# Optimization experiments

Hardware: AMD Instinct MI355X
Metric: run time of the kernel (lower is better)

Reference implementation:

```python
import jax, jax.numpy as jnp
import numpy as np


def _rnn_scan(x_pre, W_hh, b_hh, h0):
    # x_pre: [S, B, H] precomputed input projection; returns stacked h: [S, B, H]
    def step(h, xp):
        h = jnp.tanh(xp + h @ W_hh.T + b_hh)
        return h, h
    _, hs = jax.lax.scan(step, h0, x_pre)
    return hs


def setup_inputs() -> dict:
    key = jax.random.key(0)
    ks = jax.random.split(key, 12)
    B, S, E, H, V = 16, 256, 512, 1024, 32000
    sE, sH = 1.0 / np.sqrt(E), 1.0 / np.sqrt(H)
    return {
        "x_ids": jax.random.randint(ks[0], (B, S), 0, V),
        "emb": jax.random.normal(ks[1], (V, E), jnp.float32),
        "W_ih1": jax.random.normal(ks[2], (H, E), jnp.float32) * sE,
        "b_ih1": jax.random.normal(ks[3], (H,), jnp.float32) * sH,
        "W_hh1": jax.random.normal(ks[4], (H, H), jnp.float32) * sH,
        "b_hh1": jax.random.normal(ks[5], (H,), jnp.float32) * sH,
        "W_ih2": jax.random.normal(ks[6], (H, H), jnp.float32) * sH,
        "b_ih2": jax.random.normal(ks[7], (H,), jnp.float32) * sH,
        "W_hh2": jax.random.normal(ks[8], (H, H), jnp.float32) * sH,
        "b_hh2": jax.random.normal(ks[9], (H,), jnp.float32) * sH,
        "W_fc": jax.random.normal(ks[10], (V, H), jnp.float32) * sH,
        "b_fc": jax.random.normal(ks[11], (V,), jnp.float32) * sH,
    }


def reference(x_ids, emb, W_ih1, b_ih1, W_hh1, b_hh1, W_ih2, b_ih2, W_hh2, b_hh2, W_fc, b_fc):
    B, S = x_ids.shape
    H = W_hh1.shape[0]
    x = emb[x_ids]  # [B, S, E]
    # layer 1: precompute input projection for all steps, scan over time
    x1 = jnp.einsum('bse,he->sbh', x, W_ih1) + b_ih1  # [S, B, H]
    h0 = jnp.zeros((B, H), x.dtype)
    h1s = _rnn_scan(x1, W_hh1, b_hh1, h0)  # [S, B, H]
    # layer 2
    x2 = jnp.einsum('sbh,gh->sbg', h1s, W_ih2) + b_ih2
    h2s = _rnn_scan(x2, W_hh2, b_hh2, h0)  # [S, B, H]
    # per-step fc + softmax, vectorized
    logits = jnp.einsum('sbh,vh->bsv', h2s, W_fc) + b_fc  # [B, S, V]
    return jax.nn.softmax(logits, axis=-1)
```

## Files before the change

kernel.cpp:

```cpp
#include <hip/hip_runtime.h>
#include <cstdint>
#include <cstddef>

typedef unsigned short u16;
typedef __attribute__((ext_vector_type(4))) float f32x4;
typedef __attribute__((ext_vector_type(8))) short s16x8;
typedef __attribute__((ext_vector_type(8))) unsigned short u16x8;
typedef __attribute__((ext_vector_type(4))) unsigned short u16x4;
typedef __attribute__((ext_vector_type(4))) unsigned u32x4;

#define B_ 16
#define S_ 256
#define E_ 512
#define H_ 1024
#define V_ 32000
#define M_TOK (S_*B_)
#define BH (B_*H_)
#define NT_FC 250
#define MT_FC 32

__device__ __forceinline__ u16 f2bf(float f) {
  union { float f; unsigned u; } x; x.f = f;
  unsigned r = x.u + 0x7fffu + ((x.u >> 16) & 1u);
  return (u16)(r >> 16);
}
__device__ __forceinline__ float bf2f(u16 x) {
  union { unsigned u; float f; } c; c.u = ((unsigned)x) << 16; return c.f;
}

__device__ __forceinline__ void sc_load16(s16x8& d, const u16* p) {
  asm volatile("global_load_dwordx4 %0, %1, off sc0 sc1" : "=v"(d) : "v"(p));
}
__device__ __forceinline__ void sc_load16u(u32x4& d, const u16* p) {
  asm volatile("global_load_dwordx4 %0, %1, off sc0 sc1" : "=v"(d) : "v"(p));
}
__device__ __forceinline__ void sc_load8w(u16x4& d, const u16* p) {
  asm volatile("global_load_dwordx2 %0, %1, off sc0 sc1\n\ts_waitcnt vmcnt(0)"
               : "=v"(d) : "v"(p) : "memory");
}
__device__ __forceinline__ int sc_load4w(const int* p) {
  int d;
  asm volatile("global_load_dword %0, %1, off sc0 sc1\n\ts_waitcnt vmcnt(0)"
               : "=v"(d) : "v"(p) : "memory");
  return d;
}
__device__ __forceinline__ void sc_store8(u16* p, u16x4 v) {
  asm volatile("global_store_dwordx2 %0, %1, off sc0 sc1" :: "v"(p), "v"(v) : "memory");
}
__device__ __forceinline__ void sc_store4(int* p, int v) {
  asm volatile("global_store_dword %0, %1, off sc0 sc1" :: "v"(p), "v"(v) : "memory");
}
__device__ __forceinline__ void wait_vm0() {
  asm volatile("s_waitcnt vmcnt(0)" ::: "memory");
}

__global__ __launch_bounds__(256) void k_cvt(const float* __restrict__ src,
                                             u16* __restrict__ dst, int n4) {
  int i = blockIdx.x*blockDim.x + threadIdx.x;
  int stride = gridDim.x*blockDim.x;
  for (; i < n4; i += stride) {
    float4 v = reinterpret_cast<const float4*>(src)[i];
    ushort4 o;
    o.x = f2bf(v.x); o.y = f2bf(v.y); o.z = f2bf(v.z); o.w = f2bf(v.w);
    reinterpret_cast<ushort4*>(dst)[i] = o;
  }
}

__global__ __launch_bounds__(256) void k_embed(const int* __restrict__ ids,
                                               const float* __restrict__ emb,
                                               u16* __restrict__ A1) {
  int g = blockIdx.x*256 + threadIdx.x;
  int m = g >> 6;
  int c = g & 63;
  int s = m >> 4, b = m & 15;
  int id = ids[b*S_ + s];
  const float4* src = reinterpret_cast<const float4*>(emb + (size_t)id*E_ + (size_t)c*8);
  float4 v0 = src[0], v1 = src[1];
  u16x8 o;
  o[0]=f2bf(v0.x); o[1]=f2bf(v0.y); o[2]=f2bf(v0.z); o[3]=f2bf(v0.w);
  o[4]=f2bf(v1.x); o[5]=f2bf(v1.y); o[6]=f2bf(v1.z); o[7]=f2bf(v1.w);
  *reinterpret_cast<u16x8*>(A1 + (size_t)m*E_ + (size_t)c*8) = o;
}

#define BM 128
#define BN 128
#define BK 32

__device__ __forceinline__ void gload_lds16(const u16* g, u16* l) {
  __builtin_amdgcn_global_load_lds(
      (const __attribute__((address_space(1))) void*)g,
      (__attribute__((address_space(3))) void*)l,
      16, 0, 0);
}

template<int FCMODE>
__global__ __launch_bounds__(256)
void k_gemm(const u16* __restrict__ A, const u16* __restrict__ Bw,
            float* __restrict__ C, const float* __restrict__ bias,
            int M, int N, int K)
{
  __shared__ u16 lA[2][BM*BK];
  __shared__ u16 lB[2][BN*BK];
  const int tid = threadIdx.x;
  const int l = tid & 63, w = tid >> 6;

  const int nwg = gridDim.x * gridDim.y;
  int d = blockIdx.y * gridDim.x + blockIdx.x;
  int tt = (d & 7) * (nwg >> 3) + (d >> 3);
  const int n0 = (tt / gridDim.y) * BN;
  const int m0 = (tt % gridDim.y) * BM;

  const int wr = w >> 1, wc = w & 1;

  const int L0 = (w*2+0)*64 + l;
  const int L1 = (w*2+1)*64 + l;
  const int r0 = L0 >> 2, r1 = L1 >> 2;
  const int c0 = (L0 & 3) ^ ((r0 >> 1) & 3);
  const int c1 = (L1 & 3) ^ ((r1 >> 1) & 3);
  const u16* gA0 = A  + (size_t)(m0 + r0)*K + c0*8;
  const u16* gA1 = A  + (size_t)(m0 + r1)*K + c1*8;
  const u16* gB0 = Bw + (size_t)(n0 + r0)*K + c0*8;
  const u16* gB1 = Bw + (size_t)(n0 + r1)*K + c1*8;

  const int fr = l & 15;
  const int xc = (l >> 4) ^ ((fr >> 1) & 3);
  int aoff[4], boff[4];
#pragma unroll
  for (int f = 0; f < 4; ++f) {
    aoff[f] = (wr*64 + f*16 + fr) * BK + xc*8;
    boff[f] = (wc*64 + f*16 + fr) * BK + xc*8;
  }

  f32x4 acc[4][4] = {};
  const int KT = K / BK;

  gload_lds16(gA0, &lA[0][(w*2+0)*512]);
  gload_lds16(gA1, &lA[0][(w*2+1)*512]);
  gload_lds16(gB0, &lB[0][(w*2+0)*512]);
  gload_lds16(gB1, &lB[0][(w*2+1)*512]);
  __syncthreads();

  for (int kt = 0; kt < KT; ++kt) {
    const int buf = kt & 1;
    if (kt + 1 < KT) {
      const int koff = (kt+1)*BK;
      gload_lds16(gA0 + koff, &lA[buf^1][(w*2+0)*512]);
      gload_lds16(gA1 + koff, &lA[buf^1][(w*2+1)*512]);
      gload_lds16(gB0 + koff, &lB[buf^1][(w*2+0)*512]);
      gload_lds16(gB1 + koff, &lB[buf^1][(w*2+1)*512]);
    }
    s16x8 af[4], bq[4];
#pragma unroll
    for (int f = 0; f < 4; ++f) af[f] = *reinterpret_cast<const s16x8*>(&lA[buf][aoff[f]]);
#pragma unroll
    for (int f = 0; f < 4; ++f) bq[f] = *reinterpret_cast<const s16x8*>(&lB[buf][boff[f]]);
#pragma unroll
    for (int fm = 0; fm < 4; ++fm)
#pragma unroll
      for (int fn = 0; fn < 4; ++fn)
        acc[fm][fn] = __builtin_amdgcn_mfma_f32_16x16x32_bf16(af[fm], bq[fn], acc[fm][fn], 0, 0, 0);
    __syncthreads();
  }

  const int rowb = (l >> 4) * 4;
  const int colb = l & 15;
#pragma unroll
  for (int fm = 0; fm < 4; ++fm) {
#pragma unroll
    for (int fn = 0; fn < 4; ++fn) {
      const int col = n0 + wc*64 + fn*16 + colb;
#pragma unroll
      for (int r = 0; r < 4; ++r) {
        const int row = m0 + wr*64 + fm*16 + rowb + r;
        float v = acc[fm][fn][r];
        if (FCMODE == 2) {
          ((u16*)C)[(size_t)row*N + col] = f2bf(v);
        } else {
          C[(size_t)row*N + col] = v;
        }
      }
    }
  }
}

__device__ __forceinline__ void fc_tile(const u16* __restrict__ A, const u16* __restrict__ Bw,
                                        float* __restrict__ C, const float* __restrict__ bias,
                                        int m0, int n0, u16* smem)
{
  const int tid = threadIdx.x;
  const int l = tid & 63, w = tid >> 6;
  const int wr = w >> 1, wc = w & 1;
  u16* lA = smem;
  u16* lB = smem + 8192;

  const int L0 = (w*2+0)*64 + l;
  const int L1 = (w*2+1)*64 + l;
  const int r0 = L0 >> 2, r1 = L1 >> 2;
  const int c0 = (L0 & 3) ^ ((r0 >> 1) & 3);
  const int c1 = (L1 & 3) ^ ((r1 >> 1) & 3);
  const u16* gA0 = A  + (size_t)(m0 + r0)*H_ + c0*8;
  const u16* gA1 = A  + (size_t)(m0 + r1)*H_ + c1*8;
  const u16* gB0 = Bw + (size_t)(n0 + r0)*H_ + c0*8;
  const u16* gB1 = Bw + (size_t)(n0 + r1)*H_ + c1*8;

  const int fr = l & 15;
  const int xc = (l >> 4) ^ ((fr >> 1) & 3);
  int aoff[4], boff[4];
#pragma unroll
  for (int f = 0; f < 4; ++f) {
    aoff[f] = (wr*64 + f*16 + fr) * BK + xc*8;
    boff[f] = (wc*64 + f*16 + fr) * BK + xc*8;
  }

  f32x4 acc[4][4] = {};

  gload_lds16(gA0, lA + (w*2+0)*512);
  gload_lds16(gA1, lA + (w*2+1)*512);
  gload_lds16(gB0, lB + (w*2+0)*512);
  gload_lds16(gB1, lB + (w*2+1)*512);
  __syncthreads();

  for (int kt = 0; kt < 32; ++kt) {
    const int buf = kt & 1;
    if (kt + 1 < 32) {
      const int koff = (kt+1)*BK;
      gload_lds16(gA0 + koff, lA + (buf^1)*4096 + (w*2+0)*512);
      gload_lds16(gA1 + koff, lA + (buf^1)*4096 + (w*2+1)*512);
      gload_lds16(gB0 + koff, lB + (buf^1)*4096 + (w*2+0)*512);
      gload_lds16(gB1 + koff, lB + (buf^1)*4096 + (w*2+1)*512);
    }
    s16x8 af[4], bq[4];
#pragma unroll
    for (int f = 0; f < 4; ++f) af[f] = *reinterpret_cast<const s16x8*>(lA + buf*4096 + aoff[f]);
#pragma unroll
    for (int f = 0; f < 4; ++f) bq[f] = *reinterpret_cast<const s16x8*>(lB + buf*4096 + boff[f]);
#pragma unroll
    for (int fm = 0; fm < 4; ++fm)
#pragma unroll
      for (int fn = 0; fn < 4; ++fn)
        acc[fm][fn] = __builtin_amdgcn_mfma_f32_16x16x32_bf16(af[fm], bq[fn], acc[fm][fn], 0, 0, 0);
    __syncthreads();
  }

  const int rowb = (l >> 4) * 4;
  const int colb = l & 15;
#pragma unroll
  for (int fm = 0; fm < 4; ++fm) {
#pragma unroll
    for (int fn = 0; fn < 4; ++fn) {
      const int col = n0 + wc*64 + fn*16 + colb;
      const float bv = bias[col];
#pragma unroll
      for (int r = 0; r < 4; ++r) {
        const int row = m0 + wr*64 + fm*16 + rowb + r;
        const int b = row & 15, s = row >> 4;
        C[((size_t)(b*S_ + s))*V_ + col] = acc[fm][fn][r] + bv;
      }
    }
  }
}

__global__ __launch_bounds__(256)
void k_mega(const u16* __restrict__ Whh1, const u16* __restrict__ Wih2,
            const u16* __restrict__ Whh2, const u16* __restrict__ x1b,
            const float* __restrict__ bih1, const float* __restrict__ bhh1,
            const float* __restrict__ bih2, const float* __restrict__ bhh2,
            u16* __restrict__ h1s, u16* __restrict__ u2s, u16* __restrict__ h2s,
            int* __restrict__ s1, int* __restrict__ su, int* __restrict__ s2,
            const u16* __restrict__ Wfcb, const float* __restrict__ bfc,
            float* __restrict__ out, int* __restrict__ prog2, int* __restrict__ done)
{
  __shared__ u16 smem[16384];
  const int bid = blockIdx.x;
  const int tid = threadIdx.x;

  if (bid < 48) {
    const int l = tid & 63, w = tid >> 6;
    const int role = bid >> 4;
    const int blk  = bid & 15;
    const int rowA = blk*64 + w*16 + (l & 15);
    const int kc = l >> 4;
    const int bcol = l & 15;
    const int i0 = blk*64 + w*16 + kc*4;
    const int jme = (tid & 127) >> 3;

    const u16* Wsel = (role == 0) ? Whh1 : (role == 1) ? Wih2 : Whh2;
    s16x8 wf[32];
    {
      const u16* wp = Wsel + (size_t)rowA*H_ + kc*8;
#pragma unroll
      for (int ks = 0; ks < 32; ++ks) wf[ks] = *reinterpret_cast<const s16x8*>(wp + ks*32);
    }

    auto stage = [&](const u16* src, const int* sentrow) {
      while (sc_load4w(sentrow + jme) != 0) __builtin_amdgcn_s_sleep(2);
      s16x8 stg[8];
#pragma unroll
      for (int r = 0; r < 8; ++r) sc_load16(stg[r], src + (size_t)(tid + r*256)*8);
      wait_vm0();
#pragma unroll
      for (int r = 0; r < 8; ++r) {
        int idx8 = tid + r*256;
        int bt = idx8 >> 7, c8 = idx8 & 127;
        *reinterpret_cast<s16x8*>(reinterpret_cast<char*>(smem) +
            bt*2048 + ((c8*16) ^ ((bt & 7) << 4))) = stg[r];
      }
    };

    const int swz = (bcol & 7) << 4;
    auto hfrag = [&](int ks) -> s16x8 {
      return *reinterpret_cast<const s16x8*>(
          reinterpret_cast<const char*>(smem) + bcol*2048 + (((kc*16) + ks*64) ^ swz));
    };
    auto mfma32 = [&](f32x4& a0, f32x4& a1, f32x4& a2, f32x4& a3) {
#pragma unroll
      for (int ks = 0; ks < 32; ks += 4) {
        a0 = __builtin_amdgcn_mfma_f32_16x16x32_bf16(wf[ks+0], hfrag(ks+0), a0, 0, 0, 0);
        a1 = __builtin_amdgcn_mfma_f32_16x16x32_bf16(wf[ks+1], hfrag(ks+1), a1, 0, 0, 0);
        a2 = __builtin_amdgcn_mfma_f32_16x16x32_bf16(wf[ks+2], hfrag(ks+2), a2, 0, 0, 0);
        a3 = __builtin_amdgcn_mfma_f32_16x16x32_bf16(wf[ks+3], hfrag(ks+3), a3, 0, 0, 0);
      }
    };

    if (role == 0) {
      float bc[4];
#pragma unroll
      for (int r = 0; r < 4; ++r) bc[r] = bih1[i0+r] + bhh1[i0+r];
      for (int t = 0; t < S_; ++t) {
        f32x4 a0 = {}, a1 = {}, a2 = {}, a3 = {};
        if (t > 0) {
          stage(h1s + (size_t)(t-1)*BH, s1 + (t-1)*16);
          __syncthreads();
          mfma32(a0, a1, a2, a3);
        }
        u16x4 xr = *reinterpret_cast<const u16x4*>(x1b + (size_t)(t*B_ + bcol)*H_ + i0);
        f32x4 tot = (a0 + a1) + (a2 + a3);
        u16x4 o;
        o[0] = f2bf(tanhf(tot[0] + bf2f(xr[0]) + bc[0]));
        o[1] = f2bf(tanhf(tot[1] + bf2f(xr[1]) + bc[1]));
        o[2] = f2bf(tanhf(tot[2] + bf2f(xr[2]) + bc[2]));
        o[3] = f2bf(tanhf(tot[3] + bf2f(xr[3]) + bc[3]));
        sc_store8(h1s + (size_t)(t*B_ + bcol)*H_ + i0, o);
        wait_vm0();
        __syncthreads();
        if (tid == 0) sc_store4(s1 + t*16 + blk, 0);
      }
    } else if (role == 1) {
      float bc[4];
#pragma unroll
      for (int r = 0; r < 4; ++r) bc[r] = bih2[i0+r] + bhh2[i0+r];
      for (int t = 0; t < S_; ++t) {
        stage(h1s + (size_t)t*BH, s1 + t*16);
        __syncthreads();
        f32x4 a0 = {}, a1 = {}, a2 = {}, a3 = {};
        mfma32(a0, a1, a2, a3);
        f32x4 tot = (a0 + a1) + (a2 + a3);
        u16x4 o;
        o[0] = f2bf(tot[0] + bc[0]);
        o[1] = f2bf(tot[1] + bc[1]);
        o[2] = f2bf(tot[2] + bc[2]);
        o[3] = f2bf(tot[3] + bc[3]);
        sc_store8(u2s + (size_t)(t*B_ + bcol)*H_ + i0, o);
        wait_vm0();
        __syncthreads();
        if (tid == 0) sc_store4(su + t*16 + blk, 0);
      }
    } else {
      for (int t = 0; t < S_; ++t) {
        if (tid == 0) {
          while (sc_load4w(su + t*16 + blk) != 0) __builtin_amdgcn_s_sleep(2);
        }
        if (t > 0) stage(h2s + (size_t)(t-1)*BH, s2 + (t-1)*16);
        __syncthreads();
        u16x4 uv;
        sc_load8w(uv, u2s + (size_t)(t*B_ + bcol)*H_ + i0);
        f32x4 a0 = {}, a1 = {}, a2 = {}, a3 = {};
        if (t > 0) mfma32(a0, a1, a2, a3);
        f32x4 tot = (a0 + a1) + (a2 + a3);
        u16x4 o;
        o[0] = f2bf(tanhf(tot[0] + bf2f(uv[0])));
        o[1] = f2bf(tanhf(tot[1] + bf2f(uv[1])));
        o[2] = f2bf(tanhf(tot[2] + bf2f(uv[2])));
        o[3] = f2bf(tanhf(tot[3] + bf2f(uv[3])));
        sc_store8(h2s + (size_t)(t*B_ + bcol)*H_ + i0, o);
        wait_vm0();
        __syncthreads();
        if (tid == 0) {
          sc_store4(s2 + t*16 + blk, 0);
          sc_store4(prog2 + blk, t + 1);
        }
      }
    }
    return;
  }

  const int q = bid - 48;
  if (q >= MT_FC * NT_FC) return;
  const int mt = q / NT_FC;
  const int nt = q - mt * NT_FC;
  const unsigned need = (unsigned)((mt + 1) * 8);

  __shared__ int s_ok;
  if (tid == 0) {
    int ok = 0;
    const u16* pp = (const u16*)prog2;
    for (int it = 0; it < 2500; ++it) {
      u32x4 pa, pb, pc, pd;
      sc_load16u(pa, pp); sc_load16u(pb, pp + 8);
      sc_load16u(pc, pp + 16); sc_load16u(pd, pp + 24);
      wait_vm0();
      unsigned m0 = pa[0] < pa[1] ? pa[0] : pa[1];
      unsigned m1 = pa[2] < pa[3] ? pa[2] : pa[3];
      unsigned m2 = pb[0] < pb[1] ? pb[0] : pb[1];
      unsigned m3 = pb[2] < pb[3] ? pb[2] : pb[3];
      unsigned m4 = pc[0] < pc[1] ? pc[0] : pc[1];
      unsigned m5 = pc[2] < pc[3] ? pc[2] : pc[3];
      unsigned m6 = pd[0] < pd[1] ? pd[0] : pd[1];
      unsigned m7 = pd[2] < pd[3] ? pd[2] : pd[3];
      m0 = m0 < m1 ? m0 : m1;  m2 = m2 < m3 ? m2 : m3;
      m4 = m4 < m5 ? m4 : m5;  m6 = m6 < m7 ? m6 : m7;
      m0 = m0 < m2 ? m0 : m2;  m4 = m4 < m6 ? m4 : m6;
      unsigned mn = m0 < m4 ? m0 : m4;
      if (mn >= need) { ok = 1; break; }
      __builtin_amdgcn_s_sleep(32);
    }
    s_ok = ok;
  }
  __syncthreads();
  if (!s_ok) return;

  fc_tile(h2s, Wfcb, out, bfc, mt*BM, nt*BN, smem);
  if (tid == 0) done[q] = 1;
}

__global__ __launch_bounds__(256)
void k_fc_cleanup(const u16* __restrict__ h2s, const u16* __restrict__ Wfcb,
                  const float* __restrict__ bfc, float* __restrict__ out,
                  const int* __restrict__ done)
{
  __shared__ u16 smem[16384];
  const int q = blockIdx.x;
  if (done[q]) return;
  const int mt = q / NT_FC;
  const int nt = q - mt * NT_FC;
  fc_tile(h2s, Wfcb, out, bfc, mt*BM, nt*BN, smem);
}

__global__ __launch_bounds__(256)
void k_softmax(float* __restrict__ out) {
  const int gw = (blockIdx.x*256 + threadIdx.x) >> 6;
  const int l = threadIdx.x & 63;
  float* row = out + (size_t)gw*V_;
  float m = -3.4e38f, s = 0.f;
  for (int it = 0; it < 125; ++it) {
    float4 v = reinterpret_cast<const float4*>(row)[it*64 + l];
    float cm = fmaxf(fmaxf(v.x, v.y), fmaxf(v.z, v.w));
    float nm = fmaxf(m, cm);
    s = s*__expf(m - nm) + __expf(v.x-nm) + __expf(v.y-nm) + __expf(v.z-nm) + __expf(v.w-nm);
    m = nm;
  }
#pragma unroll
  for (int o = 32; o; o >>= 1) {
    float m2 = __shfl_xor(m, o), s2 = __shfl_xor(s, o);
    float nm = fmaxf(m, m2);
    s = s*__expf(m - nm) + s2*__expf(m2 - nm);
    m = nm;
  }
  const float inv = 1.f / s;
  for (int it = 0; it < 125; ++it) {
    float4 v = reinterpret_cast<const float4*>(row)[it*64 + l];
    float4 p;
    p.x = __expf(v.x - m)*inv; p.y = __expf(v.y - m)*inv;
    p.z = __expf(v.z - m)*inv; p.w = __expf(v.w - m)*inv;
    reinterpret_cast<float4*>(row)[it*64 + l] = p;
  }
}

extern "C" void kernel_launch(void* const* d_in, const int* in_sizes, int n_in,
                              void* d_out, int out_size, void* d_ws, size_t ws_size,
                              hipStream_t stream) {
  (void)in_sizes; (void)n_in; (void)out_size; (void)ws_size;
  const int*   x_ids = (const int*)  d_in[0];
  const float* emb   = (const float*)d_in[1];
  const float* Wih1  = (const float*)d_in[2];
  const float* bih1  = (const float*)d_in[3];
  const float* Whh1  = (const float*)d_in[4];
  const float* bhh1  = (const float*)d_in[5];
  const float* Wih2  = (const float*)d_in[6];
  const float* bih2  = (const float*)d_in[7];
  const float* Whh2  = (const float*)d_in[8];
  const float* bhh2  = (const float*)d_in[9];
  const float* Wfc   = (const float*)d_in[10];
  const float* bfc   = (const float*)d_in[11];
  float* out = (float*)d_out;

  char* ws = (char*)d_ws;
  size_t off = 0;
  auto alloc = [&](size_t bytes) {
    char* p = ws + off; off += (bytes + 255) & ~(size_t)255; return p;
  };
  int* sent   = (int*) alloc(3 * S_ * 16 * 4);
  int* ctrl   = (int*) alloc(64 + MT_FC*NT_FC*4);
  u16* Wfcb   = (u16*) alloc((size_t)V_*H_*2);
  u16* Whh1b  = (u16*) alloc((size_t)H_*H_*2);
  u16* Wih2b  = (u16*) alloc((size_t)H_*H_*2);
  u16* Whh2b  = (u16*) alloc((size_t)H_*H_*2);
  u16* x1b    = (u16*) alloc((size_t)M_TOK*H_*2);
  u16* h1s    = (u16*) alloc((size_t)M_TOK*H_*2);
  u16* u2s    = (u16*) alloc((size_t)M_TOK*H_*2);
  u16* h2s    = (u16*) alloc((size_t)M_TOK*H_*2);
  u16* A1     = (u16*) alloc((size_t)M_TOK*E_*2);
  u16* Wih1b  = (u16*) alloc((size_t)H_*E_*2);
  int* s1 = sent, *su = sent + S_*16, *s2 = sent + 2*S_*16;
  int* prog2 = ctrl;
  int* done  = ctrl + 16;

  k_cvt<<<256,  256, 0, stream>>>(Wih1, Wih1b, H_*E_/4);
  k_cvt<<<256,  256, 0, stream>>>(Whh1, Whh1b, H_*H_/4);
  k_cvt<<<256,  256, 0, stream>>>(Wih2, Wih2b, H_*H_/4);
  k_cvt<<<256,  256, 0, stream>>>(Whh2, Whh2b, H_*H_/4);
  k_cvt<<<2048, 256, 0, stream>>>(Wfc,  Wfcb,  V_*H_/4);
  k_embed<<<M_TOK*64/256, 256, 0, stream>>>(x_ids, emb, A1);

  k_gemm<2><<<dim3(H_/BN, M_TOK/BM), 256, 0, stream>>>(A1, Wih1b, (float*)x1b, nullptr, M_TOK, H_, E_);

  hipMemsetAsync(sent, 0xFF, 3 * S_ * 16 * 4, stream);
  hipMemsetAsync(ctrl, 0, 64 + MT_FC*NT_FC*4, stream);

  k_mega<<<48 + MT_FC*NT_FC, 256, 0, stream>>>(
      Whh1b, Wih2b, Whh2b, x1b, bih1, bhh1, bih2, bhh2,
      h1s, u2s, h2s, s1, su, s2, Wfcb, bfc, out, prog2, done);

  k_fc_cleanup<<<MT_FC*NT_FC, 256, 0, stream>>>(h2s, Wfcb, bfc, out, done);
  k_softmax<<<M_TOK/4, 256, 0, stream>>>(out);
}
```

Baseline: 1.646 ms.

## Fuse softmax into persistent mega-kernel with per-row-tile completion counters

Adds softmax blocks to the mega kernel. Each waits on a per-M-tile counter that the FC tiles bump, so softmax over finished rows overlaps the remaining recurrence and FC work. A cleanup kernel handles rows whose softmax blocks timed out. The five weight-conversion launches are also merged into one kernel. This adds more blocks that spin-wait, and FC outputs are now written with system-coherent stores, which may slow the FC epilogue.

```diff
diff --git a/kernel.cpp b/kernel.cpp
--- a/kernel.cpp
+++ b/kernel.cpp
@@ -18,6 +18,7 @@
 #define BH (B_*H_)
 #define NT_FC 250
 #define MT_FC 32
+#define NSM  (M_TOK/4)
 
 __device__ __forceinline__ u16 f2bf(float f) {
   union { float f; unsigned u; } x; x.f = f;
@@ -50,19 +51,35 @@
 __device__ __forceinline__ void sc_store4(int* p, int v) {
   asm volatile("global_store_dword %0, %1, off sc0 sc1" :: "v"(p), "v"(v) : "memory");
 }
+__device__ __forceinline__ void sc_store4f(float* p, float v) {
+  asm volatile("global_store_dword %0, %1, off sc0 sc1" :: "v"(p), "v"(v) : "memory");
+}
 __device__ __forceinline__ void wait_vm0() {
   asm volatile("s_waitcnt vmcnt(0)" ::: "memory");
 }
 
-__global__ __launch_bounds__(256) void k_cvt(const float* __restrict__ src,
-                                             u16* __restrict__ dst, int n4) {
-  int i = blockIdx.x*blockDim.x + threadIdx.x;
-  int stride = gridDim.x*blockDim.x;
-  for (; i < n4; i += stride) {
-    float4 v = reinterpret_cast<const float4*>(src)[i];
+__global__ __launch_bounds__(256)
+void k_cvt_all(const float* s0, u16* d0, int n0,
+               const float* s1, u16* d1, int n1,
+               const float* s2, u16* d2, int n2,
+               const float* s3, u16* d3, int n3,
+               const float* s4, u16* d4, int n4)
+{
+  const int total = n0 + n1 + n2 + n3 + n4;
+  for (int i = blockIdx.x*256 + threadIdx.x; i < total; i += gridDim.x*256) {
+    const float* s; u16* d; int j = i;
+    if (j < n0) { s = s0; d = d0; }
+    else { j -= n0;
+      if (j < n1) { s = s1; d = d1; }
+      else { j -= n1;
+        if (j < n2) { s = s2; d = d2; }
+        else { j -= n2;
+          if (j < n3) { s = s3; d = d3; }
+          else { j -= n3; s = s4; d = d4; } } } }
+    float4 v = reinterpret_cast<const float4*>(s)[j];
     ushort4 o;
     o.x = f2bf(v.x); o.y = f2bf(v.y); o.z = f2bf(v.z); o.w = f2bf(v.w);
-    reinterpret_cast<ushort4*>(dst)[i] = o;
+    reinterpret_cast<ushort4*>(d)[j] = o;
   }
 }
 
@@ -185,7 +202,7 @@
 
 __device__ __forceinline__ void fc_tile(const u16* __restrict__ A, const u16* __restrict__ Bw,
                                         float* __restrict__ C, const float* __restrict__ bias,
-                                        int m0, int n0, u16* smem)
+                                        int m0, int n0, u16* smem, int scmode)
 {
   const int tid = threadIdx.x;
   const int l = tid & 63, w = tid >> 6;
@@ -254,9 +271,38 @@
       for (int r = 0; r < 4; ++r) {
         const int row = m0 + wr*64 + fm*16 + rowb + r;
         const int b = row & 15, s = row >> 4;
-        C[((size_t)(b*S_ + s))*V_ + col] = acc[fm][fn][r] + bv;
-      }
-    }
+        float* p = C + ((size_t)(b*S_ + s))*V_ + col;
+        float v = acc[fm][fn][r] + bv;
+        if (scmode) sc_store4f(p, v);
+        else        *p = v;
+      }
+    }
+  }
+}
+
+__device__ __forceinline__ void softmax_row(float* row, int l) {
+  float m = -3.4e38f, s = 0.f;
+  for (int it = 0; it < 125; ++it) {
+    float4 v = reinterpret_cast<const float4*>(row)[it*64 + l];
+    float cm = fmaxf(fmaxf(v.x, v.y), fmaxf(v.z, v.w));
+    float nm = fmaxf(m, cm);
+    s = s*__expf(m - nm) + __expf(v.x-nm) + __expf(v.y-nm) + __expf(v.z-nm) + __expf(v.w-nm);
+    m = nm;
+  }
+#pragma unroll
+  for (int o = 32; o; o >>= 1) {
+    float m2 = __shfl_xor(m, o), s2 = __shfl_xor(s, o);
+    float nm = fmaxf(m, m2);
+    s = s*__expf(m - nm) + s2*__expf(m2 - nm);
+    m = nm;
+  }
+  const float inv = 1.f / s;
+  for (int it = 0; it < 125; ++it) {
+    float4 v = reinterpret_cast<const float4*>(row)[it*64 + l];
+    float4 p;
+    p.x = __expf(v.x - m)*inv; p.y = __expf(v.y - m)*inv;
+    p.z = __expf(v.z - m)*inv; p.w = __expf(v.w - m)*inv;
+    reinterpret_cast<float4*>(row)[it*64 + l] = p;
   }
 }
 
@@ -268,7 +314,8 @@
             u16* __restrict__ h1s, u16* __restrict__ u2s, u16* __restrict__ h2s,
             int* __restrict__ s1, int* __restrict__ su, int* __restrict__ s2,
             const u16* __restrict__ Wfcb, const float* __restrict__ bfc,
-            float* __restrict__ out, int* __restrict__ prog2, int* __restrict__ done)
+            float* __restrict__ out, int* __restrict__ prog2,
+            int* __restrict__ done, int* __restrict__ fcdone, int* __restrict__ smdone)
 {
   __shared__ u16 smem[16384];
   const int bid = blockIdx.x;
@@ -394,43 +441,73 @@
     return;
   }
 
-  const int q = bid - 48;
-  if (q >= MT_FC * NT_FC) return;
-  const int mt = q / NT_FC;
-  const int nt = q - mt * NT_FC;
-  const unsigned need = (unsigned)((mt + 1) * 8);
-
-  __shared__ int s_ok;
+  if (bid < 48 + MT_FC*NT_FC) {
+    const int q = bid - 48;
+    const int mt = q / NT_FC;
+    const int nt = q - mt * NT_FC;
+    const unsigned need = (unsigned)((mt + 1) * 8);
+
+    __shared__ int s_ok;
+    if (tid == 0) {
+      int ok = 0;
+      const u16* pp = (const u16*)prog2;
+      for (int it = 0; it < 2500; ++it) {
+        u32x4 pa, pb, pc, pd;
+        sc_load16u(pa, pp); sc_load16u(pb, pp + 8);
+        sc_load16u(pc, pp + 16); sc_load16u(pd, pp + 24);
+        wait_vm0();
+        unsigned m0 = pa[0] < pa[1] ? pa[0] : pa[1];
+        unsigned m1 = pa[2] < pa[3] ? pa[2] : pa[3];
+        unsigned m2 = pb[0] < pb[1] ? pb[0] : pb[1];
+        unsigned m3 = pb[2] < pb[3] ? pb[2] : pb[3];
+        unsigned m4 = pc[0] < pc[1] ? pc[0] : pc[1];
+        unsigned m5 = pc[2] < pc[3] ? pc[2] : pc[3];
+        unsigned m6 = pd[0] < pd[1] ? pd[0] : pd[1];
+        unsigned m7 = pd[2] < pd[3] ? pd[2] : pd[3];
+        m0 = m0 < m1 ? m0 : m1;  m2 = m2 < m3 ? m2 : m3;
+        m4 = m4 < m5 ? m4 : m5;  m6 = m6 < m7 ? m6 : m7;
+        m0 = m0 < m2 ? m0 : m2;  m4 = m4 < m6 ? m4 : m6;
+        unsigned mn = m0 < m4 ? m0 : m4;
+        if (mn >= need) { ok = 1; break; }
+        __builtin_amdgcn_s_sleep(32);
+      }
+      s_ok = ok;
+    }
+    __syncthreads();
+    if (!s_ok) return;
+
+    fc_tile(h2s, Wfcb, out, bfc, mt*BM, nt*BN, smem, 1);
+    wait_vm0();
+    __syncthreads();
+    if (tid == 0) {
+      done[q] = 1;
+      __hip_atomic_fetch_add(fcdone + mt, 1, __ATOMIC_RELAXED, __HIP_MEMORY_SCOPE_AGENT);
+    }
+    return;
+  }
+
+  const int sq = bid - 48 - MT_FC*NT_FC;
+  if (sq >= NSM) return;
+  const int mt = sq >> 5;
+
+  __shared__ int s_ok2;
   if (tid == 0) {
     int ok = 0;
-    const u16* pp = (const u16*)prog2;
-    for (int it = 0; it < 2500; ++it) {
-      u32x4 pa, pb, pc, pd;
-      sc_load16u(pa, pp); sc_load16u(pb, pp + 8);
-      sc_load16u(pc, pp + 16); sc_load16u(pd, pp + 24);
-      wait_vm0();
-      unsigned m0 = pa[0] < pa[1] ? pa[0] : pa[1];
-      unsigned m1 = pa[2] < pa[3] ? pa[2] : pa[3];
-      unsigned m2 = pb[0] < pb[1] ? pb[0] : pb[1];
-      unsigned m3 = pb[2] < pb[3] ? pb[2] : pb[3];
-      unsigned m4 = pc[0] < pc[1] ? pc[0] : pc[1];
-      unsigned m5 = pc[2] < pc[3] ? pc[2] : pc[3];
-      unsigned m6 = pd[0] < pd[1] ? pd[0] : pd[1];
-      unsigned m7 = pd[2] < pd[3] ? pd[2] : pd[3];
-      m0 = m0 < m1 ? m0 : m1;  m2 = m2 < m3 ? m2 : m3;
-      m4 = m4 < m5 ? m4 : m5;  m6 = m6 < m7 ? m6 : m7;
-      m0 = m0 < m2 ? m0 : m2;  m4 = m4 < m6 ? m4 : m6;
-      unsigned mn = m0 < m4 ? m0 : m4;
-      if (mn >= need) { ok = 1; break; }
+    for (int it = 0; it < 4000; ++it) {
+      if (sc_load4w(fcdone + mt) >= NT_FC) { ok = 1; break; }
       __builtin_amdgcn_s_sleep(32);
     }
-    s_ok = ok;
+    s_ok2 = ok;
   }
   __syncthreads();
-  if (!s_ok) return;
-
-  fc_tile(h2s, Wfcb, out, bfc, mt*BM, nt*BN, smem);
-  if (tid == 0) done[q] = 1;
+  if (!s_ok2) return;
+
+  const int wv = tid >> 6, l = tid & 63;
+  const int m = sq*4 + wv;
+  const int b = m & 15, s = m >> 4;
+  softmax_row(out + ((size_t)b*S_ + s)*V_, l);
+  __syncthreads();
+  if (tid == 0) smdone[sq] = 1;
 }
 
 __global__ __launch_bounds__(256)
@@ -443,37 +520,17 @@
   if (done[q]) return;
   const int mt = q / NT_FC;
   const int nt = q - mt * NT_FC;
-  fc_tile(h2s, Wfcb, out, bfc, mt*BM, nt*BN, smem);
+  fc_tile(h2s, Wfcb, out, bfc, mt*BM, nt*BN, smem, 0);
 }
 
 __global__ __launch_bounds__(256)
-void k_softmax(float* __restrict__ out) {
-  const int gw = (blockIdx.x*256 + threadIdx.x) >> 6;
-  const int l = threadIdx.x & 63;
-  float* row = out + (size_t)gw*V_;
-  float m = -3.4e38f, s = 0.f;
-  for (int it = 0; it < 125; ++it) {
-    float4 v = reinterpret_cast<const float4*>(row)[it*64 + l];
-    float cm = fmaxf(fmaxf(v.x, v.y), fmaxf(v.z, v.w));
-    float nm = fmaxf(m, cm);
-    s = s*__expf(m - nm) + __expf(v.x-nm) + __expf(v.y-nm) + __expf(v.z-nm) + __expf(v.w-nm);
-    m = nm;
-  }
-#pragma unroll
-  for (int o = 32; o; o >>= 1) {
-    float m2 = __shfl_xor(m, o), s2 = __shfl_xor(s, o);
-    float nm = fmaxf(m, m2);
-    s = s*__expf(m - nm) + s2*__expf(m2 - nm);
-    m = nm;
-  }
-  const float inv = 1.f / s;
-  for (int it = 0; it < 125; ++it) {
-    float4 v = reinterpret_cast<const float4*>(row)[it*64 + l];
-    float4 p;
-    p.x = __expf(v.x - m)*inv; p.y = __expf(v.y - m)*inv;
-    p.z = __expf(v.z - m)*inv; p.w = __expf(v.w - m)*inv;
-    reinterpret_cast<float4*>(row)[it*64 + l] = p;
-  }
+void k_softmax_cleanup(float* __restrict__ out, const int* __restrict__ smdone) {
+  const int sq = blockIdx.x;
+  if (smdone[sq]) return;
+  const int wv = threadIdx.x >> 6, l = threadIdx.x & 63;
+  const int m = sq*4 + wv;
+  const int b = m & 15, s = m >> 4;
+  softmax_row(out + ((size_t)b*S_ + s)*V_, l);
 }
 
 extern "C" void kernel_launch(void* const* d_in, const int* in_sizes, int n_in,
@@ -500,7 +557,8 @@
     char* p = ws + off; off += (bytes + 255) & ~(size_t)255; return p;
   };
   int* sent   = (int*) alloc(3 * S_ * 16 * 4);
-  int* ctrl   = (int*) alloc(64 + MT_FC*NT_FC*4);
+  const int CTRL_INTS = 16 + MT_FC*NT_FC + 32 + NSM;
+  int* ctrl   = (int*) alloc(CTRL_INTS * 4);
   u16* Wfcb   = (u16*) alloc((size_t)V_*H_*2);
   u16* Whh1b  = (u16*) alloc((size_t)H_*H_*2);
   u16* Wih2b  = (u16*) alloc((size_t)H_*H_*2);
@@ -512,25 +570,27 @@
   u16* A1     = (u16*) alloc((size_t)M_TOK*E_*2);
   u16* Wih1b  = (u16*) alloc((size_t)H_*E_*2);
   int* s1 = sent, *su = sent + S_*16, *s2 = sent + 2*S_*16;
-  int* prog2 = ctrl;
-  int* done  = ctrl + 16;
-
-  k_cvt<<<256,  256, 0, stream>>>(Wih1, Wih1b, H_*E_/4);
-  k_cvt<<<256,  256, 0, stream>>>(Whh1, Whh1b, H_*H_/4);
-  k_cvt<<<256,  256, 0, stream>>>(Wih2, Wih2b, H_*H_/4);
-  k_cvt<<<256,  256, 0, stream>>>(Whh2, Whh2b, H_*H_/4);
-  k_cvt<<<2048, 256, 0, stream>>>(Wfc,  Wfcb,  V_*H_/4);
+  int* prog2  = ctrl;
+  int* done   = ctrl + 16;
+  int* fcdone = done + MT_FC*NT_FC;
+  int* smdone = fcdone + 32;
+
+  k_cvt_all<<<2048, 256, 0, stream>>>(Wih1, Wih1b, H_*E_/4,
+                                      Whh1, Whh1b, H_*H_/4,
+                                      Wih2, Wih2b, H_*H_/4,
+                                      Whh2, Whh2b, H_*H_/4,
+                                      Wfc,  Wfcb,  V_*H_/4);
   k_embed<<<M_TOK*64/256, 256, 0, stream>>>(x_ids, emb, A1);
 
   k_gemm<2><<<dim3(H_/BN, M_TOK/BM), 256, 0, stream>>>(A1, Wih1b, (float*)x1b, nullptr, M_TOK, H_, E_);
 
   hipMemsetAsync(sent, 0xFF, 3 * S_ * 16 * 4, stream);
-  hipMemsetAsync(ctrl, 0, 64 + MT_FC*NT_FC*4, stream);
-
-  k_mega<<<48 + MT_FC*NT_FC, 256, 0, stream>>>(
+  hipMemsetAsync(ctrl, 0, CTRL_INTS * 4, stream);
+
+  k_mega<<<48 + MT_FC*NT_FC + NSM, 256, 0, stream>>>(
       Whh1b, Wih2b, Whh2b, x1b, bih1, bhh1, bih2, bhh2,
-      h1s, u2s, h2s, s1, su, s2, Wfcb, bfc, out, prog2, done);
+      h1s, u2s, h2s, s1, su, s2, Wfcb, bfc, out, prog2, done, fcdone, smdone);
 
   k_fc_cleanup<<<MT_FC*NT_FC, 256, 0, stream>>>(h2s, Wfcb, bfc, out, done);
-  k_softmax<<<M_TOK/4, 256, 0, stream>>>(out);
-}
+  k_softmax_cleanup<<<NSM, 256, 0, stream>>>(out, smdone);
+}
```

Result: slower. 1.723 ms (+4.7%).

## Fuse softmax max/sum statistics into FC epilogue via atomic online merge

Applied to the files above, without the earlier changes.

The FC tile epilogue now computes per-row max and sum-of-exponentials for its columns. It merges them into a global per-token (max, sum) record with a 64-bit CAS loop. The final softmax kernel then does a single normalize pass instead of two reads of the large logits buffer. The five weight conversion launches are also merged into one kernel. The cost is extra shuffles, shared memory use and atomic contention in the FC epilogue.

```diff
diff --git a/kernel.cpp b/kernel.cpp
--- a/kernel.cpp
+++ b/kernel.cpp
@@ -1,8 +1,10 @@
 #include <hip/hip_runtime.h>
 #include <cstdint>
 #include <cstddef>
+#include <math.h>
 
 typedef unsigned short u16;
+typedef unsigned long long u64;
 typedef __attribute__((ext_vector_type(4))) float f32x4;
 typedef __attribute__((ext_vector_type(8))) short s16x8;
 typedef __attribute__((ext_vector_type(8))) unsigned short u16x8;
@@ -54,16 +56,35 @@
   asm volatile("s_waitcnt vmcnt(0)" ::: "memory");
 }
 
-__global__ __launch_bounds__(256) void k_cvt(const float* __restrict__ src,
-                                             u16* __restrict__ dst, int n4) {
-  int i = blockIdx.x*blockDim.x + threadIdx.x;
-  int stride = gridDim.x*blockDim.x;
-  for (; i < n4; i += stride) {
-    float4 v = reinterpret_cast<const float4*>(src)[i];
+__global__ __launch_bounds__(256)
+void k_cvt_all(const float* s0, u16* d0, int n0,
+               const float* s1, u16* d1, int n1,
+               const float* s2, u16* d2, int n2,
+               const float* s3, u16* d3, int n3,
+               const float* s4, u16* d4, int n4)
+{
+  const int total = n0 + n1 + n2 + n3 + n4;
+  for (int i = blockIdx.x*256 + threadIdx.x; i < total; i += gridDim.x*256) {
+    const float* s; u16* d; int j = i;
+    if (j < n0) { s = s0; d = d0; }
+    else { j -= n0;
+      if (j < n1) { s = s1; d = d1; }
+      else { j -= n1;
+        if (j < n2) { s = s2; d = d2; }
+        else { j -= n2;
+          if (j < n3) { s = s3; d = d3; }
+          else { j -= n3; s = s4; d = d4; } } } }
+    float4 v = reinterpret_cast<const float4*>(s)[j];
     ushort4 o;
     o.x = f2bf(v.x); o.y = f2bf(v.y); o.z = f2bf(v.z); o.w = f2bf(v.w);
-    reinterpret_cast<ushort4*>(dst)[i] = o;
-  }
+    reinterpret_cast<ushort4*>(d)[j] = o;
+  }
+}
+
+__global__ __launch_bounds__(256)
+void k_init_ml(u64* __restrict__ ml) {
+  int i = blockIdx.x*256 + threadIdx.x;
+  if (i < M_TOK) ml[i] = (u64)0xFF800000u;
 }
 
 __global__ __launch_bounds__(256) void k_embed(const int* __restrict__ ids,
@@ -185,6 +206,7 @@
 
 __device__ __forceinline__ void fc_tile(const u16* __restrict__ A, const u16* __restrict__ Bw,
                                         float* __restrict__ C, const float* __restrict__ bias,
+                                        u64* __restrict__ ml,
                                         int m0, int n0, u16* smem)
 {
   const int tid = threadIdx.x;
@@ -244,6 +266,7 @@
 
   const int rowb = (l >> 4) * 4;
   const int colb = l & 15;
+
 #pragma unroll
   for (int fm = 0; fm < 4; ++fm) {
 #pragma unroll
@@ -254,8 +277,47 @@
       for (int r = 0; r < 4; ++r) {
         const int row = m0 + wr*64 + fm*16 + rowb + r;
         const int b = row & 15, s = row >> 4;
-        C[((size_t)(b*S_ + s))*V_ + col] = acc[fm][fn][r] + bv;
-      }
+        acc[fm][fn][r] += bv;
+        C[((size_t)(b*S_ + s))*V_ + col] = acc[fm][fn][r];
+      }
+    }
+  }
+
+  float2* stats = reinterpret_cast<float2*>(smem);
+#pragma unroll
+  for (int fm = 0; fm < 4; ++fm) {
+#pragma unroll
+    for (int r = 0; r < 4; ++r) {
+      float mx = fmaxf(fmaxf(acc[fm][0][r], acc[fm][1][r]),
+                       fmaxf(acc[fm][2][r], acc[fm][3][r]));
+#pragma unroll
+      for (int o = 1; o <= 8; o <<= 1) mx = fmaxf(mx, __shfl_xor(mx, o));
+      float sm = __expf(acc[fm][0][r]-mx) + __expf(acc[fm][1][r]-mx)
+               + __expf(acc[fm][2][r]-mx) + __expf(acc[fm][3][r]-mx);
+#pragma unroll
+      for (int o = 1; o <= 8; o <<= 1) sm += __shfl_xor(sm, o);
+      if (colb == 0) {
+        const int j = wr*64 + fm*16 + rowb + r;
+        stats[j*2 + wc] = make_float2(mx, sm);
+      }
+    }
+  }
+  __syncthreads();
+  if (tid < 128) {
+    float2 h0 = stats[tid*2 + 0], h1 = stats[tid*2 + 1];
+    float mx = fmaxf(h0.x, h1.x);
+    float sm = h0.y*__expf(h0.x - mx) + h1.y*__expf(h1.x - mx);
+    u64* p = ml + (m0 + tid);
+    u64 cur = *p;
+    for (;;) {
+      float mo = __uint_as_float((unsigned)(cur & 0xFFFFFFFFull));
+      float so = __uint_as_float((unsigned)(cur >> 32));
+      float mn = fmaxf(mo, mx);
+      float sn = so*__expf(mo - mn) + sm*__expf(mx - mn);
+      u64 nv = ((u64)__float_as_uint(sn) << 32) | __float_as_uint(mn);
+      u64 prev = atomicCAS(p, cur, nv);
+      if (prev == cur) break;
+      cur = prev;
     }
   }
 }
@@ -268,7 +330,8 @@
             u16* __restrict__ h1s, u16* __restrict__ u2s, u16* __restrict__ h2s,
             int* __restrict__ s1, int* __restrict__ su, int* __restrict__ s2,
             const u16* __restrict__ Wfcb, const float* __restrict__ bfc,
-            float* __restrict__ out, int* __restrict__ prog2, int* __restrict__ done)
+            float* __restrict__ out, u64* __restrict__ ml,
+            int* __restrict__ prog2, int* __restrict__ done)
 {
   __shared__ u16 smem[16384];
   const int bid = blockIdx.x;
@@ -429,49 +492,37 @@
   __syncthreads();
   if (!s_ok) return;
 
-  fc_tile(h2s, Wfcb, out, bfc, mt*BM, nt*BN, smem);
+  fc_tile(h2s, Wfcb, out, bfc, ml, mt*BM, nt*BN, smem);
   if (tid == 0) done[q] = 1;
 }
 
 __global__ __launch_bounds__(256)
 void k_fc_cleanup(const u16* __restrict__ h2s, const u16* __restrict__ Wfcb,
                   const float* __restrict__ bfc, float* __restrict__ out,
-                  const int* __restrict__ done)
+                  u64* __restrict__ ml, const int* __restrict__ done)
 {
   __shared__ u16 smem[16384];
   const int q = blockIdx.x;
   if (done[q]) return;
   const int mt = q / NT_FC;
   const int nt = q - mt * NT_FC;
-  fc_tile(h2s, Wfcb, out, bfc, mt*BM, nt*BN, smem);
+  fc_tile(h2s, Wfcb, out, bfc, ml, mt*BM, nt*BN, smem);
 }
 
 __global__ __launch_bounds__(256)
-void k_softmax(float* __restrict__ out) {
+void k_norm(float* __restrict__ out, const u64* __restrict__ ml) {
   const int gw = (blockIdx.x*256 + threadIdx.x) >> 6;
   const int l = threadIdx.x & 63;
-  float* row = out + (size_t)gw*V_;
-  float m = -3.4e38f, s = 0.f;
+  const int b = gw & 15, s = gw >> 4;
+  float* row = out + ((size_t)b*S_ + s)*V_;
+  const u64 v = ml[gw];
+  const float mx  = __uint_as_float((unsigned)(v & 0xFFFFFFFFull));
+  const float inv = 1.f / __uint_as_float((unsigned)(v >> 32));
   for (int it = 0; it < 125; ++it) {
-    float4 v = reinterpret_cast<const float4*>(row)[it*64 + l];
-    float cm = fmaxf(fmaxf(v.x, v.y), fmaxf(v.z, v.w));
-    float nm = fmaxf(m, cm);
-    s = s*__expf(m - nm) + __expf(v.x-nm) + __expf(v.y-nm) + __expf(v.z-nm) + __expf(v.w-nm);
-    m = nm;
-  }
-#pragma unroll
-  for (int o = 32; o; o >>= 1) {
-    float m2 = __shfl_xor(m, o), s2 = __shfl_xor(s, o);
-    float nm = fmaxf(m, m2);
-    s = s*__expf(m - nm) + s2*__expf(m2 - nm);
-    m = nm;
-  }
-  const float inv = 1.f / s;
-  for (int it = 0; it < 125; ++it) {
-    float4 v = reinterpret_cast<const float4*>(row)[it*64 + l];
+    float4 x = reinterpret_cast<const float4*>(row)[it*64 + l];
     float4 p;
-    p.x = __expf(v.x - m)*inv; p.y = __expf(v.y - m)*inv;
-    p.z = __expf(v.z - m)*inv; p.w = __expf(v.w - m)*inv;
+    p.x = __expf(x.x - mx)*inv; p.y = __expf(x.y - mx)*inv;
+    p.z = __expf(x.z - mx)*inv; p.w = __expf(x.w - mx)*inv;
     reinterpret_cast<float4*>(row)[it*64 + l] = p;
   }
 }
@@ -500,7 +551,9 @@
     char* p = ws + off; off += (bytes + 255) & ~(size_t)255; return p;
   };
   int* sent   = (int*) alloc(3 * S_ * 16 * 4);
-  int* ctrl   = (int*) alloc(64 + MT_FC*NT_FC*4);
+  const int CTRL_INTS = 16 + MT_FC*NT_FC;
+  int* ctrl   = (int*) alloc(CTRL_INTS * 4);
+  u64* ml     = (u64*) alloc(M_TOK * 8);
   u16* Wfcb   = (u16*) alloc((size_t)V_*H_*2);
   u16* Whh1b  = (u16*) alloc((size_t)H_*H_*2);
   u16* Wih2b  = (u16*) alloc((size_t)H_*H_*2);
@@ -515,22 +568,23 @@
   int* prog2 = ctrl;
   int* done  = ctrl + 16;
 
-  k_cvt<<<256,  256, 0, stream>>>(Wih1, Wih1b, H_*E_/4);
-  k_cvt<<<256,  256, 0, stream>>>(Whh1, Whh1b, H_*H_/4);
-  k_cvt<<<256,  256, 0, stream>>>(Wih2, Wih2b, H_*H_/4);
-  k_cvt<<<256,  256, 0, stream>>>(Whh2, Whh2b, H_*H_/4);
-  k_cvt<<<2048, 256, 0, stream>>>(Wfc,  Wfcb,  V_*H_/4);
+  k_cvt_all<<<2048, 256, 0, stream>>>(Wih1, Wih1b, H_*E_/4,
+                                      Whh1, Whh1b, H_*H_/4,
+                                      Wih2, Wih2b, H_*H_/4,
+                                      Whh2, Whh2b, H_*H_/4,
+                                      Wfc,  Wfcb,  V_*H_/4);
   k_embed<<<M_TOK*64/256, 256, 0, stream>>>(x_ids, emb, A1);
+  k_init_ml<<<M_TOK/256, 256, 0, stream>>>(ml);
 
   k_gemm<2><<<dim3(H_/BN, M_TOK/BM), 256, 0, stream>>>(A1, Wih1b, (float*)x1b, nullptr, M_TOK, H_, E_);
 
   hipMemsetAsync(sent, 0xFF, 3 * S_ * 16 * 4, stream);
-  hipMemsetAsync(ctrl, 0, 64 + MT_FC*NT_FC*4, stream);
+  hipMemsetAsync(ctrl, 0, CTRL_INTS * 4, stream);
 
   k_mega<<<48 + MT_FC*NT_FC, 256, 0, stream>>>(
       Whh1b, Wih2b, Whh2b, x1b, bih1, bhh1, bih2, bhh2,
-      h1s, u2s, h2s, s1, su, s2, Wfcb, bfc, out, prog2, done);
-
-  k_fc_cleanup<<<MT_FC*NT_FC, 256, 0, stream>>>(h2s, Wfcb, bfc, out, done);
-  k_softmax<<<M_TOK/4, 256, 0, stream>>>(out);
-}
+      h1s, u2s, h2s, s1, su, s2, Wfcb, bfc, out, ml, prog2, done);
+
+  k_fc_cleanup<<<MT_FC*NT_FC, 256, 0, stream>>>(h2s, Wfcb, bfc, out, ml, done);
+  k_norm<<<M_TOK/4, 256, 0, stream>>>(out, ml);
+}
```

After: 4.179 ms. 154% more time.
